# Optimization experiments

Hardware: AMD Instinct MI355X
Metric: run time of the kernel (lower is better)

The kernel has to match this reference:

```python
import jax, jax.numpy as jnp
import numpy as np

HEADS = 12
LN_EPS = 1e-12
NUM_PROTOTYPES = 8


def _layer_norm(x, g, b):
    mu = x.mean(-1, keepdims=True)
    var = ((x - mu) ** 2).mean(-1, keepdims=True)
    return (x - mu) / jnp.sqrt(var + LN_EPS) * g + b


def _bert_attention(q_in, kv_in, wq, bq, wk, bk, wv, bv, wo, bo, ln_g, ln_b):
    # HF BertAttention: MHA (query from q_in, key/value from kv_in) then
    # SelfOutput: dense + residual(q_in) + LayerNorm. Dropout = 0 (eval).
    B, Sq, D = q_in.shape
    Sk = kv_in.shape[1]
    dh = D // HEADS
    q = (q_in @ wq + bq).reshape(B, Sq, HEADS, dh).transpose(0, 2, 1, 3)
    k = (kv_in @ wk + bk).reshape(B, Sk, HEADS, dh).transpose(0, 2, 1, 3)
    v = (kv_in @ wv + bv).reshape(B, Sk, HEADS, dh).transpose(0, 2, 1, 3)
    scores = jnp.einsum('bhqd,bhkd->bhqk', q, k) / jnp.sqrt(jnp.asarray(dh, q.dtype))
    probs = jax.nn.softmax(scores, axis=-1)
    ctx = jnp.einsum('bhqk,bhkd->bhqd', probs, v).transpose(0, 2, 1, 3).reshape(B, Sq, D)
    return _layer_norm(ctx @ wo + bo + q_in, ln_g, ln_b)


def setup_inputs() -> dict:
    key = jax.random.key(0)
    ks = jax.random.split(key, 16)
    D = 768
    inp = {
        'local_feats': jax.random.normal(ks[0], (8, 256, D), jnp.float32),
        'global_feat_dict': jax.random.normal(ks[1], (16384, D), jnp.float32),
    }
    i = 2
    for pre in ('ll', 'lg'):
        for nm in ('wq', 'wk', 'wv', 'wo'):
            inp[f'{pre}_{nm}'] = 0.02 * jax.random.normal(ks[i], (D, D), jnp.float32)
            i += 1
        for nm in ('bq', 'bk', 'bv', 'bo'):
            inp[f'{pre}_{nm}'] = jnp.zeros((D,), jnp.float32)
        inp[f'{pre}_ln_g'] = jnp.ones((D,), jnp.float32)
        inp[f'{pre}_ln_b'] = jnp.zeros((D,), jnp.float32)
    inp['ln_g'] = jnp.ones((D,), jnp.float32)
    inp['ln_b'] = jnp.zeros((D,), jnp.float32)
    inp['aug_w'] = 0.02 * jax.random.normal(ks[i], (D, 1), jnp.float32)
    inp['ori_w'] = 0.02 * jax.random.normal(ks[i + 1], (D, 1), jnp.float32)
    inp['aug_b'] = jnp.zeros((1,), jnp.float32)
    inp['ori_b'] = jnp.zeros((1,), jnp.float32)
    return inp


def reference(local_feats, global_feat_dict,
              ll_wq, ll_bq, ll_wk, ll_bk, ll_wv, ll_bv, ll_wo, ll_bo, ll_ln_g, ll_ln_b,
              lg_wq, lg_bq, lg_wk, lg_bk, lg_wv, lg_bv, lg_wo, lg_bo, lg_ln_g, lg_ln_b,
              ln_g, ln_b, aug_w, aug_b, ori_w, ori_b):
    B, L, D = local_feats.shape
    K = NUM_PROTOTYPES
    # similarity_topk retrieval: cosine similarity against prototype pool
    g_norm = global_feat_dict / jnp.linalg.norm(global_feat_dict, axis=-1, keepdims=True)
    t_norm = local_feats / jnp.linalg.norm(local_feats, axis=-1, keepdims=True)
    sim = jnp.einsum('bld,nd->bln', t_norm, g_norm)          # [B, L, N]
    topk_idx = jax.lax.top_k(sim, K)[1]                       # [B, L, K]
    global_feats = global_feat_dict[topk_idx].reshape(B, L * K, D)
    # self-attn over locals, cross-attn locals -> retrieved prototypes
    ll = _bert_attention(local_feats, local_feats,
                         ll_wq, ll_bq, ll_wk, ll_bk, ll_wv, ll_bv, ll_wo, ll_bo, ll_ln_g, ll_ln_b)
    lg = _bert_attention(local_feats, global_feats,
                         lg_wq, lg_bq, lg_wk, lg_bk, lg_wv, lg_bv, lg_wo, lg_bo, lg_ln_g, lg_ln_b)
    out = _layer_norm(ll + lg, ln_g, ln_b)
    aug_weight = jax.nn.sigmoid(out @ aug_w + aug_b + local_feats @ ori_w + ori_b)
    return aug_weight * out + (1.0 - aug_weight) * local_feats
```

## Files before the change

### kernel.cpp

```cpp
#include <hip/hip_runtime.h>
#include <math.h>

#define D     768
#define HEADS 12
#define DH    64
#define BATCH 8
#define LSEQ  256
#define MROWS 2048
#define NDICT 16384
#define TOPK  8

typedef _Float16 half_t;
typedef half_t half8 __attribute__((ext_vector_type(8)));
typedef float floatx4 __attribute__((ext_vector_type(4)));

#define F_DICT 0u
#define F_DKV  6291456u
#define F_TN   18874368u
#define F_LOC  19660800u
#define F_WT   20447232u
#define F_BF   22806528u
#define F_TOPI 22814720u
#define F_LP   22831104u
#define F_CTX  25976832u
#define F_D1   26763264u
#define F_D3   28336128u
#define F_ML   31481856u
#define F_CANDV 31678464u
#define F_CANDI 31809536u
#define F_NRM  31940608u
#define F_USED 31956992u
#define F_ROWMAP 31973376u
#define F_INVMAP 31989760u
#define F_CNT  32006144u

typedef const __attribute__((address_space(1))) void* gptr_as1;
typedef __attribute__((address_space(3))) void* lptr_as3;
#define GLDS16(gp, lp) __builtin_amdgcn_global_load_lds((gptr_as1)(gp), (lptr_as3)(lp), 16, 0, 0)

__device__ __forceinline__ float bsum(float v, float* red) {
  int t = threadIdx.x;
  red[t] = v; __syncthreads();
  for (int s = 128; s > 0; s >>= 1) { if (t < s) red[t] += red[t + s]; __syncthreads(); }
  float r = red[0];
  __syncthreads();
  return r;
}

__global__ __launch_bounds__(256) void k_prep_wt(
    const float* __restrict__ dict, const float* __restrict__ local,
    half_t* __restrict__ gdict_h, float* __restrict__ dnrm,
    half_t* __restrict__ loc_h, half_t* __restrict__ tn_h,
    const float* w0, const float* w1, const float* w2, const float* w3,
    const float* w4, const float* w5, const float* w6, const float* w7,
    const float* b0, const float* b1, const float* b2, const float* b3,
    const float* b4, const float* b5, const float* b6, const float* b7,
    half_t* __restrict__ Wt, float* __restrict__ bfout) {
  __shared__ float red[256];
  __shared__ float tile[32][33];
  int g = blockIdx.x, t = threadIdx.x;
  if (g < NDICT) {
    const float* xr = dict + (size_t)g * D;
    float v0 = xr[t], v1 = xr[t + 256], v2 = xr[t + 512];
    float s = bsum(v0*v0 + v1*v1 + v2*v2, red);
    float n = sqrtf(s), inv = 1.0f / n;
    half_t* yr = gdict_h + (size_t)g * D;
    yr[t] = (half_t)(v0*inv); yr[t+256] = (half_t)(v1*inv); yr[t+512] = (half_t)(v2*inv);
    if (t == 0) dnrm[g] = n;
  } else if (g < NDICT + MROWS) {
    size_t r = g - NDICT;
    const float* xr = local + r * (size_t)D;
    float v0 = xr[t], v1 = xr[t + 256], v2 = xr[t + 512];
    float s = bsum(v0*v0 + v1*v1 + v2*v2, red);
    float inv = 1.0f / sqrtf(s);
    half_t* rr = loc_h + r * (size_t)D;
    half_t* nr = tn_h + r * (size_t)D;
    rr[t] = (half_t)v0;        rr[t+256] = (half_t)v1;        rr[t+512] = (half_t)v2;
    nr[t] = (half_t)(v0*inv);  nr[t+256] = (half_t)(v1*inv);  nr[t+512] = (half_t)(v2*inv);
  } else {
    const float* wsrcs[8] = {w0,w1,w2,w3,w4,w5,w6,w7};
    const float* bsrcs[8] = {b0,b1,b2,b3,b4,b5,b6,b7};
    int id = g - (NDICT + MROWS);
    int z = id / 576, rem = id % 576;
    int by = rem / 24, bx = rem % 24;
    const float* Wsrc = wsrcs[z];
    half_t* dst = Wt + (size_t)z * D * D;
    int tx = t & 31, ty = t >> 5;
    int c0 = bx * 32, r0 = by * 32;
#pragma unroll
    for (int j = 0; j < 4; j++)
      tile[ty + j*8][tx] = Wsrc[(size_t)(r0 + ty + j*8) * D + c0 + tx];
    __syncthreads();
#pragma unroll
    for (int j = 0; j < 4; j++)
      dst[(size_t)(c0 + ty + j*8) * D + r0 + tx] = (half_t)tile[tx][ty + j*8];
    if (bx == 0 && by == 0) {
#pragma unroll
      for (int j = 0; j < 3; j++)
        bfout[z * D + t + j*256] = bsrcs[z][t + j*256];
    }
  }
}

__device__ __forceinline__ void hgemm_core(
    const half_t* __restrict__ A, const half_t* __restrict__ B,
    const float* __restrict__ bias, const float* __restrict__ dnrm,
    const int* __restrict__ rowmap, void* __restrict__ Cout,
    int N, int K, int outHalf, int bx, int by, int mhalf,
    half_t* As, half_t* Bs) {
  int tid = threadIdx.x;
  int wid = tid >> 6, lane = tid & 63;
  int l16 = lane & 15, quad = lane >> 4;
  int n0 = bx * 128, m0 = by * 128;
  if (mhalf && m0 >= mhalf) { B += (size_t)D * D; if (bias) bias += D; }
  int wm = (wid & 1) * 64, wn = (wid >> 1) * 64;

  int r0  = tid >> 3;
  int cbg = (tid & 7) ^ (r0 & 7);
  const half_t* Aps[4];
#pragma unroll
  for (int i = 0; i < 4; i++) {
    int mm = m0 + r0 + 32*i;
    int mr = rowmap ? rowmap[mm] : mm;
    Aps[i] = A + (size_t)mr * K + cbg * 8;
  }
  const half_t* Bp = B + (size_t)(n0 + r0) * K + cbg * 8;

  floatx4 acc[4][4];
#pragma unroll
  for (int i = 0; i < 4; i++)
#pragma unroll
    for (int j = 0; j < 4; j++) { acc[i][j][0]=0.f; acc[i][j][1]=0.f; acc[i][j][2]=0.f; acc[i][j][3]=0.f; }

  for (int k0 = 0; k0 < K; k0 += 64) {
#pragma unroll
    for (int i = 0; i < 4; i++)
      GLDS16(Aps[i] + k0, As + ((size_t)i*256 + wid*64) * 8);
#pragma unroll
    for (int i = 0; i < 4; i++)
      GLDS16(Bp + k0 + (size_t)i * 32 * K, Bs + ((size_t)i*256 + wid*64) * 8);
    __syncthreads();
#pragma unroll
    for (int ks = 0; ks < 2; ks++) {
      half8 af[4], bf[4];
#pragma unroll
      for (int i = 0; i < 4; i++) {
        int row = wm + i*16 + l16;
        int cb = (quad + ks*4) ^ (row & 7);
        af[i] = *(const half8*)&As[row*64 + cb*8];
      }
#pragma unroll
      for (int j = 0; j < 4; j++) {
        int row = wn + j*16 + l16;
        int cb = (quad + ks*4) ^ (row & 7);
        bf[j] = *(const half8*)&Bs[row*64 + cb*8];
      }
#pragma unroll
      for (int i = 0; i < 4; i++)
#pragma unroll
        for (int j = 0; j < 4; j++)
          acc[i][j] = __builtin_amdgcn_mfma_f32_16x16x32_f16(af[i], bf[j], acc[i][j], 0, 0, 0);
    }
    __syncthreads();
  }

  float bcol[4];
#pragma unroll
  for (int j = 0; j < 4; j++) bcol[j] = bias ? bias[n0 + wn + j*16 + l16] : 0.f;
  if (outHalf) {
    half_t* C = (half_t*)Cout;
#pragma unroll
    for (int i = 0; i < 4; i++)
#pragma unroll
      for (int r = 0; r < 4; r++) {
        int grow = m0 + wm + i*16 + quad*4 + r;
        float sc = dnrm ? dnrm[rowmap ? rowmap[grow] : grow] : 1.0f;
#pragma unroll
        for (int j = 0; j < 4; j++)
          C[(size_t)grow * N + n0 + wn + j*16 + l16] = (half_t)(acc[i][j][r] * sc + bcol[j]);
      }
  } else {
    float* C = (float*)Cout;
#pragma unroll
    for (int i = 0; i < 4; i++)
#pragma unroll
      for (int r = 0; r < 4; r++) {
        int grow = m0 + wm + i*16 + quad*4 + r;
        float sc = dnrm ? dnrm[rowmap ? rowmap[grow] : grow] : 1.0f;
#pragma unroll
        for (int j = 0; j < 4; j++)
          C[(size_t)grow * N + n0 + wn + j*16 + l16] = acc[i][j][r] * sc + bcol[j];
      }
  }
}

__global__ __launch_bounds__(256) void k_gemm_simlp(
    const half_t* __restrict__ tn, const half_t* __restrict__ gd,
    half_t* __restrict__ sim,
    const half_t* __restrict__ loc, const half_t* __restrict__ wt0,
    const float* __restrict__ bf0, half_t* __restrict__ lp) {
  __shared__ half_t As[128*64];
  __shared__ half_t Bs[128*64];
  int gid = blockIdx.x;
  if (gid < 2048) {
    int bx = (gid & 7) + ((gid >> 3) / 16) * 8;
    int by = (gid >> 3) % 16;
    hgemm_core(tn, gd, nullptr, nullptr, nullptr, sim, NDICT, D, 1, bx, by, 0, As, Bs);
  } else {
    int rel = gid - 2048;
    int bx = (rel & 7) + ((rel >> 3) / 16) * 8;
    int by = (rel >> 3) % 16;
    hgemm_core(loc, wt0, bf0, nullptr, nullptr, lp, 3072, D, 1, bx, by, 0, As, Bs);
  }
}

__global__ __launch_bounds__(256) void k_gemm_dkv(
    const half_t* __restrict__ gd, const half_t* __restrict__ wt4,
    const float* __restrict__ bf4, const float* __restrict__ dnrm,
    const int* __restrict__ rowmap, const int* __restrict__ cnt,
    half_t* __restrict__ dkv) {
  __shared__ half_t As[128*64];
  __shared__ half_t Bs[128*64];
  int mceil = (*cnt + 127) & ~127;
  if ((int)blockIdx.y * 128 >= mceil) return;
  hgemm_core(gd, wt4, bf4, dnrm, rowmap, dkv, 1536, D, 1, blockIdx.x, blockIdx.y, 0, As, Bs);
}

__global__ __launch_bounds__(256) void k_gemm_wo(
    const half_t* __restrict__ ctx, const half_t* __restrict__ wt6,
    const float* __restrict__ bf6, float* __restrict__ dd) {
  __shared__ half_t As[128*64];
  __shared__ half_t Bs[128*64];
  hgemm_core(ctx, wt6, bf6, nullptr, nullptr, dd, D, D, 0, blockIdx.x, blockIdx.y, MROWS, As, Bs);
}

__global__ __launch_bounds__(256) void k_topk1(const half_t* __restrict__ sim,
                                               float* __restrict__ candv,
                                               int* __restrict__ candi,
                                               int* __restrict__ used,
                                               int* __restrict__ rowmap,
                                               int* __restrict__ cnt) {
  int t = threadIdx.x;
  if (t < 4) used[blockIdx.x * 4 + t] = 0;
  else if (t < 8) rowmap[blockIdx.x * 4 + t - 4] = 0;
  if (blockIdx.x == 0 && t == 8) *cnt = 0;

  int gw = blockIdx.x * 4 + (t >> 6);
  int lane = t & 63;
  int row = gw >> 3, seg = gw & 7;
  int cbase = seg * 2048;
  const half_t* p = sim + (size_t)row * NDICT + cbase;

  float v[32];
#pragma unroll
  for (int i = 0; i < 4; i++) {
    half8 h = *(const half8*)(p + i*512 + lane*8);
#pragma unroll
    for (int j = 0; j < 8; j++) v[i*8 + j] = (float)h[j];
  }
  float m = v[0]; int pos = 0;
#pragma unroll
  for (int i = 1; i < 32; i++) { if (v[i] > m) { m = v[i]; pos = i; } }

  for (int it = 0; it < 8; it++) {
    int gidx = cbase + (pos >> 3) * 512 + lane * 8 + (pos & 7);
    float bv = m; int bi = gidx;
#pragma unroll
    for (int d2 = 1; d2 < 64; d2 <<= 1) {
      float ov = __shfl_xor(bv, d2); int oi = __shfl_xor(bi, d2);
      if (ov > bv || (ov == bv && oi < bi)) { bv = ov; bi = oi; }
    }
    if (lane == 0) {
      size_t base = (size_t)row * 64 + seg * 8 + it;
      candv[base] = bv; candi[base] = bi;
    }
    if (bi == gidx) {
      v[pos] = -INFINITY;
      m = v[0]; pos = 0;
#pragma unroll
      for (int i = 1; i < 32; i++) { if (v[i] > m) { m = v[i]; pos = i; } }
    }
  }
}

__global__ __launch_bounds__(256) void k_topk2(const float* __restrict__ candv,
                                               const int* __restrict__ candi,
                                               int* __restrict__ topi) {
  int row = blockIdx.x * 4 + (threadIdx.x >> 6);
  int lane = threadIdx.x & 63;
  float v = candv[(size_t)row * 64 + lane];
  int id = candi[(size_t)row * 64 + lane];
#pragma unroll
  for (int it = 0; it < 8; it++) {
    float bv = v; int bi = id;
#pragma unroll
    for (int d2 = 1; d2 < 64; d2 <<= 1) {
      float ov = __shfl_xor(bv, d2); int oi = __shfl_xor(bi, d2);
      if (ov > bv || (ov == bv && oi < bi)) { bv = ov; bi = oi; }
    }
    if (lane == 0) topi[row * 8 + it] = bi;
    if (id == bi) { v = -INFINITY; id = 0x7FFFFFFF; }
  }
}

__global__ __launch_bounds__(256) void k_mark(const int* __restrict__ topi,
                                              int* __restrict__ used) {
  int i = blockIdx.x * 256 + threadIdx.x;
  used[topi[i]] = 1;
}
__global__ __launch_bounds__(256) void k_cmp(const int* __restrict__ used,
                                             int* __restrict__ rowmap,
                                             int* __restrict__ invmap,
                                             int* __restrict__ cnt) {
  int i = blockIdx.x * 256 + threadIdx.x;
  if (used[i]) { int s = atomicAdd(cnt, 1); rowmap[s] = i; invmap[i] = s; }
}
__global__ __launch_bounds__(256) void k_remap(int* __restrict__ topi,
                                               const int* __restrict__ invmap) {
  int i = blockIdx.x * 256 + threadIdx.x;
  topi[i] = invmap[topi[i]];
}

__global__ __launch_bounds__(256) void k_flash2(
    const half_t* __restrict__ lp, const half_t* __restrict__ dkv,
    const int* __restrict__ topi_,
    half_t* __restrict__ ctx_ll, half_t* __restrict__ Opart, float* __restrict__ ml) {
  __shared__ half_t Ks[64][72];
  __shared__ half_t Vt[64][72];
  __shared__ half_t Ps[4][16][72];

  int tid = threadIdx.x;
  int wid = tid >> 6;
  int lane = tid & 63;
  int l16 = lane & 15, quad = lane >> 4;

  const half_t *Q, *K, *V; const int* kidx; half_t* Out;
  int qS, kvS, Sk, ns, rel;
  if (blockIdx.x < BATCH*HEADS*4*4) {
    rel = blockIdx.x;
    Q = lp + 2304; qS = 3072; K = dkv; V = dkv + 768; kvS = 1536;
    kidx = topi_; Sk = LSEQ*TOPK; ns = 4; Out = nullptr;
  } else {
    rel = blockIdx.x - BATCH*HEADS*4*4;
    Q = lp; qS = 3072; K = lp + 768; V = lp + 1536; kvS = 3072;
    kidx = nullptr; Sk = LSEQ; ns = 1; Out = ctx_ll;
  }

  int sp = rel % ns;
  int rest = rel / ns;
  int qt = rest & 3;
  int h  = (rest >> 2) % HEADS;
  int bb = rest / (4 * HEADS);
  int q0 = qt * 64 + wid * 16;
  int sLen = Sk / ns, s0 = sp * sLen;

  const float SCL = 0.125f * 1.4426950408889634f;
  const half_t* qrow = Q + (size_t)(bb * LSEQ + q0 + l16) * qS + h * DH;
  half8 aq0 = *(const half8*)(qrow + quad*8);
  half8 aq1 = *(const half8*)(qrow + 32 + quad*8);

  floatx4 o[4];
#pragma unroll
  for (int nt = 0; nt < 4; nt++) { o[nt][0]=0.f; o[nt][1]=0.f; o[nt][2]=0.f; o[nt][3]=0.f; }
  float mreg[4] = {-INFINITY, -INFINITY, -INFINITY, -INFINITY};
  float lreg[4] = {0.f, 0.f, 0.f, 0.f};

  for (int k0 = s0; k0 < s0 + sLen; k0 += 64) {
    {
      int row = tid >> 2, cg = tid & 3;
      int key = k0 + row;
      size_t rowid = kidx ? (size_t)kidx[(size_t)bb * Sk + key]
                          : (size_t)(bb * LSEQ + key);
      const half_t* kb = K + rowid * (size_t)kvS + h * DH + cg * 16;
      const half_t* vb = V + rowid * (size_t)kvS + h * DH + cg * 16;
      *(half8*)&Ks[row][cg*16]     = *(const half8*)kb;
      *(half8*)&Ks[row][cg*16 + 8] = *(const half8*)(kb + 8);
      half8 v0 = *(const half8*)vb, v1 = *(const half8*)(vb + 8);
#pragma unroll
      for (int jj = 0; jj < 8; jj++) { Vt[cg*16 + jj][row] = v0[jj]; Vt[cg*16 + 8 + jj][row] = v1[jj]; }
    }
    __syncthreads();

    floatx4 c[4];
#pragma unroll
    for (int nt = 0; nt < 4; nt++) {
      half8 b0 = *(const half8*)&Ks[nt*16 + l16][quad*8];
      half8 b1 = *(const half8*)&Ks[nt*16 + l16][32 + quad*8];
      floatx4 z; z[0]=0.f; z[1]=0.f; z[2]=0.f; z[3]=0.f;
      z = __builtin_amdgcn_mfma_f32_16x16x32_f16(aq0, b0, z, 0, 0, 0);
      z = __builtin_amdgcn_mfma_f32_16x16x32_f16(aq1, b1, z, 0, 0, 0);
      c[nt] = z;
    }

    float alpha[4];
#pragma unroll
    for (int r = 0; r < 4; r++) {
      float mx = fmaxf(fmaxf(c[0][r], c[1][r]), fmaxf(c[2][r], c[3][r]));
      mx = fmaxf(mx, __shfl_xor(mx, 1));
      mx = fmaxf(mx, __shfl_xor(mx, 2));
      mx = fmaxf(mx, __shfl_xor(mx, 4));
      mx = fmaxf(mx, __shfl_xor(mx, 8));
      float mn = fmaxf(mreg[r], mx);
      float al = __builtin_amdgcn_exp2f((mreg[r] - mn) * SCL);
      float ps = 0.f;
#pragma unroll
      for (int nt = 0; nt < 4; nt++) {
        float p = __builtin_amdgcn_exp2f((c[nt][r] - mn) * SCL);
        c[nt][r] = p; ps += p;
      }
      ps += __shfl_xor(ps, 1);
      ps += __shfl_xor(ps, 2);
      ps += __shfl_xor(ps, 4);
      ps += __shfl_xor(ps, 8);
      mreg[r] = mn; lreg[r] = lreg[r] * al + ps; alpha[r] = al;
    }

#pragma unroll
    for (int nt = 0; nt < 4; nt++)
#pragma unroll
      for (int r = 0; r < 4; r++)
        Ps[wid][quad*4 + r][nt*16 + l16] = (half_t)c[nt][r];
    half8 p0 = *(const half8*)&Ps[wid][l16][quad*8];
    half8 p1 = *(const half8*)&Ps[wid][l16][32 + quad*8];

#pragma unroll
    for (int nt = 0; nt < 4; nt++)
#pragma unroll
      for (int r = 0; r < 4; r++) o[nt][r] *= alpha[r];
#pragma unroll
    for (int nt = 0; nt < 4; nt++) {
      half8 v0 = *(const half8*)&Vt[nt*16 + l16][quad*8];
      half8 v1 = *(const half8*)&Vt[nt*16 + l16][32 + quad*8];
      o[nt] = __builtin_amdgcn_mfma_f32_16x16x32_f16(p0, v0, o[nt], 0, 0, 0);
      o[nt] = __builtin_amdgcn_mfma_f32_16x16x32_f16(p1, v1, o[nt], 0, 0, 0);
    }
    __syncthreads();
  }

  if (ns == 1) {
    half_t* ob = Out + (size_t)(bb * LSEQ + q0 + quad*4) * D + h * DH;
#pragma unroll
    for (int r = 0; r < 4; r++) {
      float inv = 1.0f / lreg[r];
#pragma unroll
      for (int nt = 0; nt < 4; nt++)
        ob[(size_t)r * D + nt*16 + l16] = (half_t)(o[nt][r] * inv);
    }
  } else {
    size_t rbase = (size_t)sp * MROWS + bb * LSEQ + q0 + quad*4;
    half_t* ob = Opart + rbase * D + h * DH;
#pragma unroll
    for (int r = 0; r < 4; r++) {
      float inv = 1.0f / lreg[r];
#pragma unroll
      for (int nt = 0; nt < 4; nt++)
        ob[(size_t)r * D + nt*16 + l16] = (half_t)(o[nt][r] * inv);
    }
    if (l16 == 0) {
#pragma unroll
      for (int r = 0; r < 4; r++) {
        size_t mi = ((rbase + r) * HEADS + h) * 2;
        ml[mi] = mreg[r]; ml[mi + 1] = lreg[r];
      }
    }
  }
}

__global__ __launch_bounds__(256) void k_comb(const half_t* __restrict__ Op,
                                              const float* __restrict__ ml,
                                              half_t* __restrict__ ctx) {
  int r = blockIdx.x, t = threadIdx.x;
  const float SCL = 0.125f * 1.4426950408889634f;
#pragma unroll
  for (int i = 0; i < 3; i++) {
    int col = t + i*256;
    int h = col >> 6;
    float m[4], l[4];
    float ms = -INFINITY;
#pragma unroll
    for (int s = 0; s < 4; s++) {
      size_t mi = (((size_t)s * MROWS + r) * HEADS + h) * 2;
      m[s] = ml[mi]; l[s] = ml[mi + 1];
      ms = fmaxf(ms, m[s]);
    }
    float den = 0.f, num = 0.f;
#pragma unroll
    for (int s = 0; s < 4; s++) {
      float w = __builtin_amdgcn_exp2f((m[s] - ms) * SCL) * l[s];
      den += w;
      num += w * (float)Op[((size_t)s * MROWS + r) * D + col];
    }
    ctx[(size_t)r * D + col] = (half_t)(num / den);
  }
}

__global__ __launch_bounds__(256) void k_lngate3(
    const float* __restrict__ dd, const float* __restrict__ loc,
    const float* __restrict__ llg, const float* __restrict__ llb,
    const float* __restrict__ lgg, const float* __restrict__ lgb,
    const float* __restrict__ lng, const float* __restrict__ lnb,
    const float* __restrict__ aw, const float* __restrict__ ow,
    const float* __restrict__ ab, const float* __restrict__ orb,
    float* __restrict__ y) {
  __shared__ float red[256];
  size_t r = blockIdx.x; int t = threadIdx.x;
  const float* ar = dd + r*(size_t)D;
  const float* br = dd + ((size_t)MROWS + r)*(size_t)D;
  const float* lcl = loc + r*(size_t)D;
  float l0 = lcl[t], l1 = lcl[t+256], l2 = lcl[t+512];

  float a0 = ar[t]+l0, a1 = ar[t+256]+l1, a2 = ar[t+512]+l2;
  float mu = bsum(a0+a1+a2, red) * (1.0f/768.0f);
  float d0 = a0-mu, d1 = a1-mu, d2 = a2-mu;
  float var = bsum(d0*d0 + d1*d1 + d2*d2, red) * (1.0f/768.0f);
  float rstd = rsqrtf(var + 1e-12f);
  float x0 = d0*rstd*llg[t]     + llb[t];
  float x1 = d1*rstd*llg[t+256] + llb[t+256];
  float x2 = d2*rstd*llg[t+512] + llb[t+512];

  float b0 = br[t]+l0, b1 = br[t+256]+l1, b2 = br[t+512]+l2;
  mu = bsum(b0+b1+b2, red) * (1.0f/768.0f);
  d0 = b0-mu; d1 = b1-mu; d2 = b2-mu;
  var = bsum(d0*d0 + d1*d1 + d2*d2, red) * (1.0f/768.0f);
  rstd = rsqrtf(var + 1e-12f);
  x0 += d0*rstd*lgg[t]     + lgb[t];
  x1 += d1*rstd*lgg[t+256] + lgb[t+256];
  x2 += d2*rstd*lgg[t+512] + lgb[t+512];

  mu = bsum(x0+x1+x2, red) * (1.0f/768.0f);
  d0 = x0-mu; d1 = x1-mu; d2 = x2-mu;
  var = bsum(d0*d0 + d1*d1 + d2*d2, red) * (1.0f/768.0f);
  rstd = rsqrtf(var + 1e-12f);
  float o0 = d0*rstd*lng[t]     + lnb[t];
  float o1 = d1*rstd*lng[t+256] + lnb[t+256];
  float o2 = d2*rstd*lng[t+512] + lnb[t+512];

  float s = o0*aw[t] + l0*ow[t]
          + o1*aw[t+256] + l1*ow[t+256]
          + o2*aw[t+512] + l2*ow[t+512];
  float z = bsum(s, red) + ab[0] + orb[0];
  float w = 1.0f / (1.0f + __expf(-z));
  float* yr = y + r*(size_t)D;
  yr[t]     = w*o0 + (1.f-w)*l0;
  yr[t+256] = w*o1 + (1.f-w)*l1;
  yr[t+512] = w*o2 + (1.f-w)*l2;
}

extern "C" void kernel_launch(void* const* d_in, const int* in_sizes, int n_in,
                              void* d_out, int out_size, void* d_ws, size_t ws_size,
                              hipStream_t stream) {
  (void)in_sizes; (void)n_in; (void)out_size; (void)ws_size;
  const float* local = (const float*)d_in[0];
  const float* dict  = (const float*)d_in[1];
  const float* ll_g  = (const float*)d_in[10];
  const float* ll_b  = (const float*)d_in[11];
  const float* lg_g  = (const float*)d_in[20];
  const float* lg_b  = (const float*)d_in[21];
  const float* ln_g  = (const float*)d_in[22];
  const float* ln_b  = (const float*)d_in[23];
  const float* aug_w = (const float*)d_in[24];
  const float* ori_w = (const float*)d_in[25];
  const float* aug_b = (const float*)d_in[26];
  const float* ori_b = (const float*)d_in[27];

  float* W = (float*)d_ws;
  half_t* gdict_h = (half_t*)(W + F_DICT);
  half_t* sim_h   = (half_t*)(W + F_DKV);
  half_t* dkv     = (half_t*)(W + F_DKV);
  half_t* tn_h    = (half_t*)(W + F_TN);
  half_t* loc_h   = (half_t*)(W + F_LOC);
  half_t* wt      = (half_t*)(W + F_WT);
  float*  bf      = W + F_BF;
  int*    topi    = (int*)(W + F_TOPI);
  half_t* lp      = (half_t*)(W + F_LP);
  half_t* ctx_ll  = (half_t*)(W + F_CTX);
  half_t* ctx_lg  = (half_t*)(W + F_D1);
  half_t* Opart   = (half_t*)(W + F_D1);
  float*  dd      = W + F_D3;
  float*  ml      = W + F_ML;
  float*  candv   = W + F_CANDV;
  int*    candi   = (int*)(W + F_CANDI);
  float*  dnrm    = W + F_NRM;
  int*    used    = (int*)(W + F_USED);
  int*    rowmap  = (int*)(W + F_ROWMAP);
  int*    invmap  = (int*)(W + F_INVMAP);
  int*    cnt     = (int*)(W + F_CNT);

  dim3 blk(256);
  const size_t WS = (size_t)D * D;

  k_prep_wt<<<NDICT + MROWS + 4608, blk, 0, stream>>>(
      dict, local, gdict_h, dnrm, loc_h, tn_h,
      (const float*)d_in[2], (const float*)d_in[3], (const float*)d_in[4],
      (const float*)d_in[12], (const float*)d_in[13], (const float*)d_in[14],
      (const float*)d_in[5], (const float*)d_in[15],
      (const float*)d_in[6], (const float*)d_in[7], (const float*)d_in[8],
      (const float*)d_in[16], (const float*)d_in[17], (const float*)d_in[18],
      (const float*)d_in[9], (const float*)d_in[19], wt, bf);

  k_gemm_simlp<<<2048 + 384, blk, 0, stream>>>(tn_h, gdict_h, sim_h,
                                               loc_h, wt + 0*WS, bf + 0, lp);

  k_topk1<<<MROWS*8/4, blk, 0, stream>>>(sim_h, candv, candi, used, rowmap, cnt);
  k_topk2<<<MROWS/4, blk, 0, stream>>>(candv, candi, topi);
  k_mark<<<64, blk, 0, stream>>>(topi, used);
  k_cmp<<<64, blk, 0, stream>>>(used, rowmap, invmap, cnt);
  k_remap<<<64, blk, 0, stream>>>(topi, invmap);

  k_gemm_dkv<<<dim3(12, 128), blk, 0, stream>>>(
      gdict_h, wt + 4*WS, bf + 3072, dnrm, rowmap, cnt, dkv);

  k_flash2<<<dim3(BATCH*HEADS*4*4 + BATCH*HEADS*4), blk, 0, stream>>>(
      lp, dkv, topi, ctx_ll, Opart, ml);
  k_comb<<<MROWS, blk, 0, stream>>>(Opart, ml, ctx_lg);

  k_gemm_wo<<<dim3(6, 32), blk, 0, stream>>>(ctx_ll, wt + 6*WS, bf + 4608, dd);

  k_lngate3<<<MROWS, blk, 0, stream>>>(dd, local,
      ll_g, ll_b, lg_g, lg_b, ln_g, ln_b,
      aug_w, ori_w, aug_b, ori_b, (float*)d_out);
}
```

Before: 436.1 us.

## Process all query tiles per flash block to reuse K/V loads, fuse mark into topk2

Each flash-attention block now handles all four 64-row query tiles for its (batch, head, split), so the gathered K/V tile staged in shared memory is reused four times instead of being reloaded by four separate blocks. The grid shrinks from 1920 to 480 blocks, with an XCD-style swizzle of the block index. The separate k_mark launch is folded into k_topk2, which now sets the used flags directly. The trade-off is much higher register pressure (16 accumulators plus running max and sum per thread) and fewer blocks, which can reduce occupancy and parallelism on a large GPU.

```diff
diff --git a/kernel.cpp b/kernel.cpp
--- a/kernel.cpp
+++ b/kernel.cpp
@@ -285,7 +285,8 @@
 
 __global__ __launch_bounds__(256) void k_topk2(const float* __restrict__ candv,
                                                const int* __restrict__ candi,
-                                               int* __restrict__ topi) {
+                                               int* __restrict__ topi,
+                                               int* __restrict__ used) {
   int row = blockIdx.x * 4 + (threadIdx.x >> 6);
   int lane = threadIdx.x & 63;
   float v = candv[(size_t)row * 64 + lane];
@@ -298,16 +299,11 @@
       float ov = __shfl_xor(bv, d2); int oi = __shfl_xor(bi, d2);
       if (ov > bv || (ov == bv && oi < bi)) { bv = ov; bi = oi; }
     }
-    if (lane == 0) topi[row * 8 + it] = bi;
+    if (lane == 0) { topi[row * 8 + it] = bi; used[bi] = 1; }
     if (id == bi) { v = -INFINITY; id = 0x7FFFFFFF; }
   }
 }
 
-__global__ __launch_bounds__(256) void k_mark(const int* __restrict__ topi,
-                                              int* __restrict__ used) {
-  int i = blockIdx.x * 256 + threadIdx.x;
-  used[topi[i]] = 1;
-}
 __global__ __launch_bounds__(256) void k_cmp(const int* __restrict__ used,
                                              int* __restrict__ rowmap,
                                              int* __restrict__ invmap,
@@ -334,36 +330,42 @@
   int lane = tid & 63;
   int l16 = lane & 15, quad = lane >> 4;
 
+  int gid = blockIdx.x;
+  int swz = (gid & 7) * 60 + (gid >> 3);
+
   const half_t *Q, *K, *V; const int* kidx; half_t* Out;
-  int qS, kvS, Sk, ns, rel;
-  if (blockIdx.x < BATCH*HEADS*4*4) {
-    rel = blockIdx.x;
-    Q = lp + 2304; qS = 3072; K = dkv; V = dkv + 768; kvS = 1536;
+  int kvS, Sk, ns, sp, h, bb;
+  if (swz < 384) {
+    sp = swz & 3; int rest = swz >> 2;
+    h = rest % HEADS; bb = rest / HEADS;
+    Q = lp + 2304; K = dkv; V = dkv + 768; kvS = 1536;
     kidx = topi_; Sk = LSEQ*TOPK; ns = 4; Out = nullptr;
   } else {
-    rel = blockIdx.x - BATCH*HEADS*4*4;
-    Q = lp; qS = 3072; K = lp + 768; V = lp + 1536; kvS = 3072;
+    int rel = swz - 384;
+    sp = 0; h = rel % HEADS; bb = rel / HEADS;
+    Q = lp; K = lp + 768; V = lp + 1536; kvS = 3072;
     kidx = nullptr; Sk = LSEQ; ns = 1; Out = ctx_ll;
   }
-
-  int sp = rel % ns;
-  int rest = rel / ns;
-  int qt = rest & 3;
-  int h  = (rest >> 2) % HEADS;
-  int bb = rest / (4 * HEADS);
-  int q0 = qt * 64 + wid * 16;
   int sLen = Sk / ns, s0 = sp * sLen;
 
   const float SCL = 0.125f * 1.4426950408889634f;
-  const half_t* qrow = Q + (size_t)(bb * LSEQ + q0 + l16) * qS + h * DH;
-  half8 aq0 = *(const half8*)(qrow + quad*8);
-  half8 aq1 = *(const half8*)(qrow + 32 + quad*8);
-
-  floatx4 o[4];
-#pragma unroll
-  for (int nt = 0; nt < 4; nt++) { o[nt][0]=0.f; o[nt][1]=0.f; o[nt][2]=0.f; o[nt][3]=0.f; }
-  float mreg[4] = {-INFINITY, -INFINITY, -INFINITY, -INFINITY};
-  float lreg[4] = {0.f, 0.f, 0.f, 0.f};
+  half8 aq[4][2];
+#pragma unroll
+  for (int qt = 0; qt < 4; qt++) {
+    const half_t* qrow = Q + (size_t)(bb * LSEQ + qt*64 + wid*16 + l16) * 3072 + h * DH;
+    aq[qt][0] = *(const half8*)(qrow + quad*8);
+    aq[qt][1] = *(const half8*)(qrow + 32 + quad*8);
+  }
+
+  floatx4 o[4][4];
+  float mreg[4][4], lreg[4][4];
+#pragma unroll
+  for (int qt = 0; qt < 4; qt++)
+#pragma unroll
+    for (int nt = 0; nt < 4; nt++) {
+      o[qt][nt][0]=0.f; o[qt][nt][1]=0.f; o[qt][nt][2]=0.f; o[qt][nt][3]=0.f;
+      mreg[qt][nt] = -INFINITY; lreg[qt][nt] = 0.f;
+    }
 
   for (int k0 = s0; k0 < s0 + sLen; k0 += 64) {
     {
@@ -381,86 +383,95 @@
     }
     __syncthreads();
 
-    floatx4 c[4];
-#pragma unroll
-    for (int nt = 0; nt < 4; nt++) {
-      half8 b0 = *(const half8*)&Ks[nt*16 + l16][quad*8];
-      half8 b1 = *(const half8*)&Ks[nt*16 + l16][32 + quad*8];
-      floatx4 z; z[0]=0.f; z[1]=0.f; z[2]=0.f; z[3]=0.f;
-      z = __builtin_amdgcn_mfma_f32_16x16x32_f16(aq0, b0, z, 0, 0, 0);
-      z = __builtin_amdgcn_mfma_f32_16x16x32_f16(aq1, b1, z, 0, 0, 0);
-      c[nt] = z;
-    }
-
-    float alpha[4];
-#pragma unroll
-    for (int r = 0; r < 4; r++) {
-      float mx = fmaxf(fmaxf(c[0][r], c[1][r]), fmaxf(c[2][r], c[3][r]));
-      mx = fmaxf(mx, __shfl_xor(mx, 1));
-      mx = fmaxf(mx, __shfl_xor(mx, 2));
-      mx = fmaxf(mx, __shfl_xor(mx, 4));
-      mx = fmaxf(mx, __shfl_xor(mx, 8));
-      float mn = fmaxf(mreg[r], mx);
-      float al = __builtin_amdgcn_exp2f((mreg[r] - mn) * SCL);
-      float ps = 0.f;
+#pragma unroll
+    for (int qt = 0; qt < 4; qt++) {
+      floatx4 c[4];
 #pragma unroll
       for (int nt = 0; nt < 4; nt++) {
-        float p = __builtin_amdgcn_exp2f((c[nt][r] - mn) * SCL);
-        c[nt][r] = p; ps += p;
-      }
-      ps += __shfl_xor(ps, 1);
-      ps += __shfl_xor(ps, 2);
-      ps += __shfl_xor(ps, 4);
-      ps += __shfl_xor(ps, 8);
-      mreg[r] = mn; lreg[r] = lreg[r] * al + ps; alpha[r] = al;
-    }
-
-#pragma unroll
-    for (int nt = 0; nt < 4; nt++)
-#pragma unroll
-      for (int r = 0; r < 4; r++)
-        Ps[wid][quad*4 + r][nt*16 + l16] = (half_t)c[nt][r];
-    half8 p0 = *(const half8*)&Ps[wid][l16][quad*8];
-    half8 p1 = *(const half8*)&Ps[wid][l16][32 + quad*8];
-
-#pragma unroll
-    for (int nt = 0; nt < 4; nt++)
-#pragma unroll
-      for (int r = 0; r < 4; r++) o[nt][r] *= alpha[r];
-#pragma unroll
-    for (int nt = 0; nt < 4; nt++) {
-      half8 v0 = *(const half8*)&Vt[nt*16 + l16][quad*8];
-      half8 v1 = *(const half8*)&Vt[nt*16 + l16][32 + quad*8];
-      o[nt] = __builtin_amdgcn_mfma_f32_16x16x32_f16(p0, v0, o[nt], 0, 0, 0);
-      o[nt] = __builtin_amdgcn_mfma_f32_16x16x32_f16(p1, v1, o[nt], 0, 0, 0);
+        half8 b0 = *(const half8*)&Ks[nt*16 + l16][quad*8];
+        half8 b1 = *(const half8*)&Ks[nt*16 + l16][32 + quad*8];
+        floatx4 z; z[0]=0.f; z[1]=0.f; z[2]=0.f; z[3]=0.f;
+        z = __builtin_amdgcn_mfma_f32_16x16x32_f16(aq[qt][0], b0, z, 0, 0, 0);
+        z = __builtin_amdgcn_mfma_f32_16x16x32_f16(aq[qt][1], b1, z, 0, 0, 0);
+        c[nt] = z;
+      }
+
+      float alpha[4];
+#pragma unroll
+      for (int r = 0; r < 4; r++) {
+        float mx = fmaxf(fmaxf(c[0][r], c[1][r]), fmaxf(c[2][r], c[3][r]));
+        mx = fmaxf(mx, __shfl_xor(mx, 1));
+        mx = fmaxf(mx, __shfl_xor(mx, 2));
+        mx = fmaxf(mx, __shfl_xor(mx, 4));
+        mx = fmaxf(mx, __shfl_xor(mx, 8));
+        float mn = fmaxf(mreg[qt][r], mx);
+        float al = __builtin_amdgcn_exp2f((mreg[qt][r] - mn) * SCL);
+        float ps = 0.f;
+#pragma unroll
+        for (int nt = 0; nt < 4; nt++) {
+          float p = __builtin_amdgcn_exp2f((c[nt][r] - mn) * SCL);
+          c[nt][r] = p; ps += p;
+        }
+        ps += __shfl_xor(ps, 1);
+        ps += __shfl_xor(ps, 2);
+        ps += __shfl_xor(ps, 4);
+        ps += __shfl_xor(ps, 8);
+        mreg[qt][r] = mn; lreg[qt][r] = lreg[qt][r] * al + ps; alpha[r] = al;
+      }
+
+#pragma unroll
+      for (int nt = 0; nt < 4; nt++)
+#pragma unroll
+        for (int r = 0; r < 4; r++)
+          Ps[wid][quad*4 + r][nt*16 + l16] = (half_t)c[nt][r];
+      half8 p0 = *(const half8*)&Ps[wid][l16][quad*8];
+      half8 p1 = *(const half8*)&Ps[wid][l16][32 + quad*8];
+
+#pragma unroll
+      for (int nt = 0; nt < 4; nt++)
+#pragma unroll
+        for (int r = 0; r < 4; r++) o[qt][nt][r] *= alpha[r];
+#pragma unroll
+      for (int nt = 0; nt < 4; nt++) {
+        half8 v0 = *(const half8*)&Vt[nt*16 + l16][quad*8];
+        half8 v1 = *(const half8*)&Vt[nt*16 + l16][32 + quad*8];
+        o[qt][nt] = __builtin_amdgcn_mfma_f32_16x16x32_f16(p0, v0, o[qt][nt], 0, 0, 0);
+        o[qt][nt] = __builtin_amdgcn_mfma_f32_16x16x32_f16(p1, v1, o[qt][nt], 0, 0, 0);
+      }
     }
     __syncthreads();
   }
 
   if (ns == 1) {
-    half_t* ob = Out + (size_t)(bb * LSEQ + q0 + quad*4) * D + h * DH;
-#pragma unroll
-    for (int r = 0; r < 4; r++) {
-      float inv = 1.0f / lreg[r];
-#pragma unroll
-      for (int nt = 0; nt < 4; nt++)
-        ob[(size_t)r * D + nt*16 + l16] = (half_t)(o[nt][r] * inv);
+#pragma unroll
+    for (int qt = 0; qt < 4; qt++) {
+      half_t* ob = Out + (size_t)(bb * LSEQ + qt*64 + wid*16 + quad*4) * D + h * DH;
+#pragma unroll
+      for (int r = 0; r < 4; r++) {
+        float inv = 1.0f / lreg[qt][r];
+#pragma unroll
+        for (int nt = 0; nt < 4; nt++)
+          ob[(size_t)r * D + nt*16 + l16] = (half_t)(o[qt][nt][r] * inv);
+      }
     }
   } else {
-    size_t rbase = (size_t)sp * MROWS + bb * LSEQ + q0 + quad*4;
-    half_t* ob = Opart + rbase * D + h * DH;
-#pragma unroll
-    for (int r = 0; r < 4; r++) {
-      float inv = 1.0f / lreg[r];
-#pragma unroll
-      for (int nt = 0; nt < 4; nt++)
-        ob[(size_t)r * D + nt*16 + l16] = (half_t)(o[nt][r] * inv);
-    }
-    if (l16 == 0) {
+#pragma unroll
+    for (int qt = 0; qt < 4; qt++) {
+      size_t rbase = (size_t)sp * MROWS + bb * LSEQ + qt*64 + wid*16 + quad*4;
+      half_t* ob = Opart + rbase * D + h * DH;
 #pragma unroll
       for (int r = 0; r < 4; r++) {
-        size_t mi = ((rbase + r) * HEADS + h) * 2;
-        ml[mi] = mreg[r]; ml[mi + 1] = lreg[r];
+        float inv = 1.0f / lreg[qt][r];
+#pragma unroll
+        for (int nt = 0; nt < 4; nt++)
+          ob[(size_t)r * D + nt*16 + l16] = (half_t)(o[qt][nt][r] * inv);
+      }
+      if (l16 == 0) {
+#pragma unroll
+        for (int r = 0; r < 4; r++) {
+          size_t mi = ((rbase + r) * HEADS + h) * 2;
+          ml[mi] = mreg[qt][r]; ml[mi + 1] = lreg[qt][r];
+        }
       }
     }
   }
@@ -602,15 +613,14 @@
                                                loc_h, wt + 0*WS, bf + 0, lp);
 
   k_topk1<<<MROWS*8/4, blk, 0, stream>>>(sim_h, candv, candi, used, rowmap, cnt);
-  k_topk2<<<MROWS/4, blk, 0, stream>>>(candv, candi, topi);
-  k_mark<<<64, blk, 0, stream>>>(topi, used);
+  k_topk2<<<MROWS/4, blk, 0, stream>>>(candv, candi, topi, used);
   k_cmp<<<64, blk, 0, stream>>>(used, rowmap, invmap, cnt);
   k_remap<<<64, blk, 0, stream>>>(topi, invmap);
 
   k_gemm_dkv<<<dim3(12, 128), blk, 0, stream>>>(
       gdict_h, wt + 4*WS, bf + 3072, dnrm, rowmap, cnt, dkv);
 
-  k_flash2<<<dim3(BATCH*HEADS*4*4 + BATCH*HEADS*4), blk, 0, stream>>>(
+  k_flash2<<<dim3(480), blk, 0, stream>>>(
       lp, dkv, topi, ctx_ll, Opart, ml);
   k_comb<<<MROWS, blk, 0, stream>>>(Opart, ml, ctx_lg);
 
```

Result: slower. 446.9 us (+2.5%).
